# Kernel tuning notes

Hardware: AMD Instinct MI355X
Metric: run time of the kernel (lower is better)

## Reference

```python
import jax, jax.numpy as jnp
import numpy as np

T, N, E = 12, 100000, 3200000
F = H = 64
O, L = 32, 2


def setup_inputs() -> dict:
    key = jax.random.key(0)
    ks = jax.random.split(key, 13)
    sc = 0.08  # keep gate pre-activations in a sane range
    return {
        "x": jax.random.normal(ks[0], (T, N, F), jnp.float32),
        "hidden_states": jax.random.normal(ks[1], (L, N, H), jnp.float32),
        "cell_states": jax.random.normal(ks[2], (L, N, H), jnp.float32),
        "Wx_self": jax.random.normal(ks[3], (L, 4, F, H), jnp.float32) * sc,
        "Wx_neigh": jax.random.normal(ks[4], (L, 4, F, H), jnp.float32) * sc,
        "Wh_self": jax.random.normal(ks[5], (L, 4, H, H), jnp.float32) * sc,
        "Wh_neigh": jax.random.normal(ks[6], (L, 4, H, H), jnp.float32) * sc,
        "w_c": jax.random.normal(ks[7], (L, 3, H), jnp.float32) * sc,  # peephole i,f,o
        "bias": jax.random.normal(ks[8], (L, 4, H), jnp.float32) * sc,  # i,f,c,o
        "Wout": jax.random.normal(ks[9], (H, O), jnp.float32) * sc,
        "bout": jax.random.normal(ks[10], (O,), jnp.float32) * sc,
        "src": jax.random.randint(ks[11], (E,), 0, N, jnp.int32),
        "dst": jax.random.randint(ks[12], (E,), 0, N, jnp.int32),
    }


def reference(x, hidden_states, cell_states, Wx_self, Wx_neigh, Wh_self,
              Wh_neigh, w_c, bias, Wout, bout, src, dst):
    # mean aggregation over incoming edges (DGL copy_u + mean reduce)
    deg = jax.ops.segment_sum(jnp.ones((E,), x.dtype), dst, num_segments=N)
    deg_inv = jnp.where(deg > 0, 1.0 / deg, 0.0)[:, None]  # [N,1]

    def mean_agg(feat):  # [N,D] -> [N,D]
        return jax.ops.segment_sum(feat[src], dst, num_segments=N) * deg_inv

    def gates(feat, agg, Ws, Wn):  # Ws,Wn: [4,D,H] -> [4,N,H]
        return (jnp.einsum('nf,gfh->gnh', feat, Ws)
                + jnp.einsum('nf,gfh->gnh', agg, Wn))

    def step(carry, x_t):
        hs, cs = carry  # [L,N,H] each
        inp = x_t
        new_h, new_c = [], []
        for j in range(L):
            h, c = hs[j], cs[j]
            x_agg = mean_agg(inp)  # reuse_msg_passing: one agg shared by 4 gates
            h_agg = mean_agg(h)
            pre = gates(inp, x_agg, Wx_self[j], Wx_neigh[j]) \
                + gates(h, h_agg, Wh_self[j], Wh_neigh[j])  # [4,N,H]
            i = jax.nn.sigmoid(pre[0] + w_c[j, 0] * c + bias[j, 0])
            f = jax.nn.sigmoid(pre[1] + w_c[j, 1] * c + bias[j, 1])
            c_tilde = jnp.tanh(pre[2] + bias[j, 2])
            nc = f * c + i * c_tilde
            o = jax.nn.sigmoid(pre[3] + w_c[j, 2] * nc + bias[j, 3])
            nh = o * jnp.tanh(nc)
            new_h.append(nh)
            new_c.append(nc)
            inp = nh
        out_t = inp @ Wout + bout  # [N,O]
        return (jnp.stack(new_h), jnp.stack(new_c)), out_t

    (h_f, c_f), outs = jax.lax.scan(step, (hidden_states, cell_states), x)
    return outs, h_f, c_f  # outs: [T,N,O]
```

## Files before the change

kernel.cpp:

```cpp
#include <hip/hip_runtime.h>

#define T_STEPS 12
#define NN 100000
#define EE 3200000
#define HD 64
#define OD 32
#define NBK 391

typedef __attribute__((ext_vector_type(8))) short short8;
typedef __attribute__((ext_vector_type(4))) float f32x4;
typedef __attribute__((ext_vector_type(2))) float f32x2;
typedef unsigned short u16;
typedef unsigned char u8;

__device__ __forceinline__ u16 f2b(float x) {
  union { float f; unsigned u; } v; v.f = x;
  unsigned r = v.u + 0x7FFFu + ((v.u >> 16) & 1u);
  return (u16)(r >> 16);
}
__device__ __forceinline__ u16 f2h(float x) {
  union { _Float16 h; u16 s; } u; u.h = (_Float16)x; return u.s;
}
__device__ __forceinline__ float h2f(u16 s) {
  union { u16 s; _Float16 h; } u; u.s = s; return (float)u.h;
}
__device__ __forceinline__ float sigm(float x) {
  x = fminf(fmaxf(x, -30.f), 30.f);
  return 1.0f / (1.0f + __expf(-x));
}
__device__ __forceinline__ float tanh_f(float x) {
  x = fminf(fmaxf(x, -15.f), 15.f);
  float e = __expf(2.0f * x);
  return (e - 1.0f) / (e + 1.0f);
}

__device__ __forceinline__ uint2 pack8_fp8(const float* f) {
  unsigned lo = 0, hi = 0;
  lo = __builtin_amdgcn_cvt_pk_fp8_f32(f[0], f[1], lo, false);
  lo = __builtin_amdgcn_cvt_pk_fp8_f32(f[2], f[3], lo, true);
  hi = __builtin_amdgcn_cvt_pk_fp8_f32(f[4], f[5], hi, false);
  hi = __builtin_amdgcn_cvt_pk_fp8_f32(f[6], f[7], hi, true);
  return make_uint2(lo, hi);
}
__device__ __forceinline__ u8 f2q(float x) {
  return (u8)(__builtin_amdgcn_cvt_pk_fp8_f32(x, 0.f, 0u, false) & 0xFFu);
}
__device__ __forceinline__ void acc8_fp8(uint2 v, float* a) {
  f32x2 p0 = __builtin_amdgcn_cvt_pk_f32_fp8(v.x, false);
  f32x2 p1 = __builtin_amdgcn_cvt_pk_f32_fp8(v.x, true);
  f32x2 p2 = __builtin_amdgcn_cvt_pk_f32_fp8(v.y, false);
  f32x2 p3 = __builtin_amdgcn_cvt_pk_f32_fp8(v.y, true);
  a[0] += p0[0]; a[1] += p0[1]; a[2] += p1[0]; a[3] += p1[1];
  a[4] += p2[0]; a[5] += p2[1]; a[6] += p3[0]; a[7] += p3[1];
}
__device__ __forceinline__ void dec16_acc2(uint4 q, f32x2* a) {
  a[0] += __builtin_amdgcn_cvt_pk_f32_fp8(q.x, false);
  a[1] += __builtin_amdgcn_cvt_pk_f32_fp8(q.x, true);
  a[2] += __builtin_amdgcn_cvt_pk_f32_fp8(q.y, false);
  a[3] += __builtin_amdgcn_cvt_pk_f32_fp8(q.y, true);
  a[4] += __builtin_amdgcn_cvt_pk_f32_fp8(q.z, false);
  a[5] += __builtin_amdgcn_cvt_pk_f32_fp8(q.z, true);
  a[6] += __builtin_amdgcn_cvt_pk_f32_fp8(q.w, false);
  a[7] += __builtin_amdgcn_cvt_pk_f32_fp8(q.w, true);
}
__device__ __forceinline__ short8 s8_from_fp8(uint2 q) {
  f32x2 p0 = __builtin_amdgcn_cvt_pk_f32_fp8(q.x, false);
  f32x2 p1 = __builtin_amdgcn_cvt_pk_f32_fp8(q.x, true);
  f32x2 p2 = __builtin_amdgcn_cvt_pk_f32_fp8(q.y, false);
  f32x2 p3 = __builtin_amdgcn_cvt_pk_f32_fp8(q.y, true);
  short8 o;
  o[0] = (short)f2b(p0[0]); o[1] = (short)f2b(p0[1]);
  o[2] = (short)f2b(p1[0]); o[3] = (short)f2b(p1[1]);
  o[4] = (short)f2b(p2[0]); o[5] = (short)f2b(p2[1]);
  o[6] = (short)f2b(p3[0]); o[7] = (short)f2b(p3[1]);
  return o;
}
__device__ __forceinline__ short8 s8_from_f32(float4 a, float4 b) {
  short8 o;
  o[0] = (short)f2b(a.x); o[1] = (short)f2b(a.y);
  o[2] = (short)f2b(a.z); o[3] = (short)f2b(a.w);
  o[4] = (short)f2b(b.x); o[5] = (short)f2b(b.y);
  o[6] = (short)f2b(b.z); o[7] = (short)f2b(b.w);
  return o;
}

__global__ __launch_bounds__(256) void k_bhist(const int* __restrict__ dst,
                                               int* __restrict__ bcnt, int E) {
  __shared__ int h[NBK];
  for (int i = threadIdx.x; i < NBK; i += 256) h[i] = 0;
  __syncthreads();
  int base = blockIdx.x * 4096;
#pragma unroll
  for (int i = 0; i < 16; ++i) {
    int e = base + i * 256 + threadIdx.x;
    if (e < E) atomicAdd(&h[dst[e] >> 8], 1);
  }
  __syncthreads();
  for (int i = threadIdx.x; i < NBK; i += 256)
    if (h[i]) atomicAdd(&bcnt[i], h[i]);
}

__global__ __launch_bounds__(512) void k_bscan(const int* __restrict__ bcnt,
                                               int* __restrict__ bcur) {
  __shared__ int buf[512];
  int tid = threadIdx.x;
  int v = (tid < NBK) ? bcnt[tid] : 0;
  buf[tid] = v;
  __syncthreads();
  for (int off = 1; off < 512; off <<= 1) {
    int t = (tid >= off) ? buf[tid - off] : 0;
    __syncthreads();
    buf[tid] += t;
    __syncthreads();
  }
  if (tid < NBK) bcur[tid] = buf[tid] - v;
}

__global__ __launch_bounds__(256) void k_bscatter(const int* __restrict__ src,
                                                  const int* __restrict__ dst,
                                                  int* __restrict__ bcur,
                                                  uint2* __restrict__ binned, int E) {
  __shared__ int h[NBK];
  __shared__ int base[NBK];
  __shared__ int cur[NBK];
  for (int i = threadIdx.x; i < NBK; i += 256) { h[i] = 0; cur[i] = 0; }
  __syncthreads();
  int b0 = blockIdx.x * 4096;
  int d[16], s[16];
#pragma unroll
  for (int i = 0; i < 16; ++i) {
    int e = b0 + i * 256 + threadIdx.x;
    if (e < E) {
      d[i] = dst[e];
      s[i] = src[e];
      atomicAdd(&h[d[i] >> 8], 1);
    } else d[i] = -1;
  }
  __syncthreads();
  for (int i = threadIdx.x; i < NBK; i += 256)
    if (h[i]) base[i] = atomicAdd(&bcur[i], h[i]);
  __syncthreads();
#pragma unroll
  for (int i = 0; i < 16; ++i) {
    if (d[i] >= 0) {
      int bk = d[i] >> 8;
      int r = atomicAdd(&cur[bk], 1);
      binned[base[bk] + r] = make_uint2((unsigned)s[i], (unsigned)d[i]);
    }
  }
}

__global__ __launch_bounds__(256) void k_count2(const uint2* __restrict__ binned,
                                                int* __restrict__ deg, int E) {
  int e = blockIdx.x * 256 + threadIdx.x;
  if (e < E) atomicAdd(&deg[binned[e].y], 1);
}

__global__ __launch_bounds__(1024) void k_scanA(const int* __restrict__ deg,
                                                int* __restrict__ excl,
                                                int* __restrict__ btot, int n) {
  __shared__ int buf[1024];
  int tid = threadIdx.x;
  int i = blockIdx.x * 1024 + tid;
  int v = (i < n) ? deg[i] : 0;
  buf[tid] = v;
  __syncthreads();
  for (int off = 1; off < 1024; off <<= 1) {
    int t = (tid >= off) ? buf[tid - off] : 0;
    __syncthreads();
    buf[tid] += t;
    __syncthreads();
  }
  if (i < n) excl[i] = buf[tid] - v;
  if (tid == 1023) btot[blockIdx.x] = buf[1023];
}

__global__ __launch_bounds__(128) void k_scanB(const int* __restrict__ btot,
                                               int* __restrict__ boffs, int nb) {
  __shared__ int buf[128];
  int tid = threadIdx.x;
  int v = (tid < nb) ? btot[tid] : 0;
  buf[tid] = v;
  __syncthreads();
  for (int off = 1; off < 128; off <<= 1) {
    int t = (tid >= off) ? buf[tid - off] : 0;
    __syncthreads();
    buf[tid] += t;
    __syncthreads();
  }
  if (tid < nb) boffs[tid] = buf[tid] - v;
}

__global__ __launch_bounds__(1024) void k_scanC(const int* __restrict__ deg,
                                                const int* __restrict__ excl,
                                                const int* __restrict__ boffs,
                                                int* __restrict__ row_ptr,
                                                int* __restrict__ cursor,
                                                float* __restrict__ deg_inv, int n) {
  int i = blockIdx.x * 1024 + threadIdx.x;
  if (i < n) {
    int v = excl[i] + boffs[blockIdx.x];
    int d = deg[i];
    row_ptr[i] = v;
    cursor[i] = v;
    deg_inv[i] = d ? (1.0f / (float)d) : 0.0f;
    if (i == n - 1) row_ptr[n] = v + d;
  }
}

__global__ __launch_bounds__(256) void k_scatter2(const uint2* __restrict__ binned,
                                                  int* __restrict__ cursor,
                                                  int* __restrict__ csr, int E) {
  int e = blockIdx.x * 256 + threadIdx.x;
  if (e < E) {
    uint2 p = binned[e];
    int pos = atomicAdd(&cursor[p.y], 1);
    csr[pos] = (int)p.x;
  }
}

__global__ __launch_bounds__(256) void k_prep(const float* __restrict__ Wxs,
                                              const float* __restrict__ Wxn,
                                              const float* __restrict__ Whs,
                                              const float* __restrict__ Whn,
                                              u16* __restrict__ bprep) {
  int idx = blockIdx.x * 256 + threadIdx.x;
  int l = idx >> 16;
  int kb = (idx >> 13) & 7;
  int fi = (idx >> 9) & 15;
  int ln = (idx >> 3) & 63;
  int j = idx & 7;
  int fc = kb * 32 + ((ln >> 4) << 3) + j;
  int g = fi & 3;
  int kk = ((fi >> 2) << 4) + (ln & 15);
  int t = fc >> 6, f = fc & 63;
  const float* tabs[4] = {Wxs, Wxn, Whs, Whn};
  bprep[idx] = f2b(tabs[t][((size_t)(l * 4 + g) * 64 + f) * 64 + kk]);
}

__global__ __launch_bounds__(256) void k_prepw(const float* __restrict__ Wout,
                                               u16* __restrict__ wp) {
  int idx = blockIdx.x * 256 + threadIdx.x;
  int kb = idx >> 10;
  int fi = (idx >> 9) & 1;
  int ln = (idx >> 3) & 63;
  int j = idx & 7;
  int k = kb * 32 + ((ln >> 4) << 3) + j;
  int o = fi * 16 + (ln & 15);
  wp[idx] = f2b(Wout[k * 32 + o]);
}

__global__ __launch_bounds__(256) void k_convxall(const float* __restrict__ x,
                                                  u8* __restrict__ XQ) {
  int tid = blockIdx.x * 256 + threadIdx.x;
  int j = tid & 7;
  int tn = tid >> 3;
  int n = tn % NN;
  int t = tn / NN;
  const float* rp = x + (size_t)tn * 64 + j * 8;
  float4 v0 = *reinterpret_cast<const float4*>(rp);
  float4 v1 = *reinterpret_cast<const float4*>(rp + 4);
  float f[8] = {v0.x, v0.y, v0.z, v0.w, v1.x, v1.y, v1.z, v1.w};
  *reinterpret_cast<uint2*>(XQ + (size_t)n * 768 + t * 64 + j * 8) = pack8_fp8(f);
}

__global__ __launch_bounds__(256) void k_inith(const float* __restrict__ h0,
                                               const float* __restrict__ c0,
                                               u16* __restrict__ H0bf,
                                               u16* __restrict__ L1bf,
                                               u8* __restrict__ HQ,
                                               u16* __restrict__ C16) {
  int idx = blockIdx.x * 256 + threadIdx.x;
  int n = idx >> 3, j = idx & 7;
#pragma unroll
  for (int L = 0; L < 2; ++L) {
    const float* rp = h0 + (size_t)L * NN * 64 + (size_t)n * 64 + j * 8;
    float4 v0 = *reinterpret_cast<const float4*>(rp);
    float4 v1 = *reinterpret_cast<const float4*>(rp + 4);
    float f[8] = {v0.x, v0.y, v0.z, v0.w, v1.x, v1.y, v1.z, v1.w};
    short8 o;
#pragma unroll
    for (int i = 0; i < 8; ++i) o[i] = (short)f2b(f[i]);
    if (L == 0)
      *reinterpret_cast<short8*>(H0bf + (size_t)n * 64 + j * 8) = o;
    else
      *reinterpret_cast<short8*>(L1bf + (size_t)n * 64 + j * 8) = o;
    *reinterpret_cast<uint2*>(HQ + (size_t)n * 128 + L * 64 + j * 8) = pack8_fp8(f);
    const float* cp = c0 + (size_t)L * NN * 64 + (size_t)n * 64 + j * 8;
    float4 c0v = *reinterpret_cast<const float4*>(cp);
    float4 c1v = *reinterpret_cast<const float4*>(cp + 4);
    float cf[8] = {c0v.x, c0v.y, c0v.z, c0v.w, c1v.x, c1v.y, c1v.z, c1v.w};
    short8 oc;
#pragma unroll
    for (int i = 0; i < 8; ++i) oc[i] = (short)f2h(cf[i]);
    *reinterpret_cast<short8*>(C16 + (size_t)L * NN * 64 + (size_t)n * 64 + j * 8) = oc;
  }
}

__global__ __launch_bounds__(256) void k_aggx(const u8* __restrict__ XQ,
                                              const int* __restrict__ row_ptr,
                                              const int* __restrict__ csr,
                                              const float* __restrict__ deg_inv,
                                              u8* __restrict__ AGGXq) {
  int node = blockIdx.x * 4 + (threadIdx.x >> 6);
  int lane = threadIdx.x & 63;
  int g = lane >> 4, m = lane & 15;
  int start = row_ptr[node], end = row_ptr[node + 1];
  f32x2 acc[3][8];
#pragma unroll
  for (int p = 0; p < 3; ++p)
#pragma unroll
    for (int i = 0; i < 8; ++i) acc[p][i] = (f32x2){0.f, 0.f};
  int e = start + g;
  for (; e + 4 < end; e += 8) {
    int s0 = csr[e], s1 = csr[e + 4];
    const u8* r0 = XQ + (size_t)s0 * 768 + m * 16;
    const u8* r1 = XQ + (size_t)s1 * 768 + m * 16;
#pragma unroll
    for (int p = 0; p < 3; ++p) {
      uint4 q0 = *reinterpret_cast<const uint4*>(r0 + p * 256);
      uint4 q1 = *reinterpret_cast<const uint4*>(r1 + p * 256);
      dec16_acc2(q0, acc[p]);
      dec16_acc2(q1, acc[p]);
    }
  }
  if (e < end) {
    int s0 = csr[e];
    const u8* r0 = XQ + (size_t)s0 * 768 + m * 16;
#pragma unroll
    for (int p = 0; p < 3; ++p) {
      uint4 q0 = *reinterpret_cast<const uint4*>(r0 + p * 256);
      dec16_acc2(q0, acc[p]);
    }
  }
#pragma unroll
  for (int off = 16; off < 64; off <<= 1)
#pragma unroll
    for (int p = 0; p < 3; ++p)
#pragma unroll
      for (int i = 0; i < 8; ++i) {
        acc[p][i][0] += __shfl_xor(acc[p][i][0], off);
        acc[p][i][1] += __shfl_xor(acc[p][i][1], off);
      }
  if (g == 0) {
    float sc = deg_inv[node];
#pragma unroll
    for (int p = 0; p < 3; ++p) {
      float f[16];
#pragma unroll
      for (int i = 0; i < 8; ++i) {
        f[i * 2] = acc[p][i][0] * sc;
        f[i * 2 + 1] = acc[p][i][1] * sc;
      }
      uint4 o;
      unsigned w;
      w = 0; w = __builtin_amdgcn_cvt_pk_fp8_f32(f[0], f[1], w, false);
      w = __builtin_amdgcn_cvt_pk_fp8_f32(f[2], f[3], w, true); o.x = w;
      w = 0; w = __builtin_amdgcn_cvt_pk_fp8_f32(f[4], f[5], w, false);
      w = __builtin_amdgcn_cvt_pk_fp8_f32(f[6], f[7], w, true); o.y = w;
      w = 0; w = __builtin_amdgcn_cvt_pk_fp8_f32(f[8], f[9], w, false);
      w = __builtin_amdgcn_cvt_pk_fp8_f32(f[10], f[11], w, true); o.z = w;
      w = 0; w = __builtin_amdgcn_cvt_pk_fp8_f32(f[12], f[13], w, false);
      w = __builtin_amdgcn_cvt_pk_fp8_f32(f[14], f[15], w, true); o.w = w;
      int t = p * 4 + (m >> 2);
      *reinterpret_cast<uint4*>(AGGXq + ((size_t)t * NN + node) * 64 + (m & 3) * 16) = o;
    }
  }
}

__global__ __launch_bounds__(256) void k_agg_pair(const u8* __restrict__ Q,
                                                  const int* __restrict__ row_ptr,
                                                  const int* __restrict__ csr,
                                                  const float* __restrict__ deg_inv,
                                                  u16* __restrict__ out0,
                                                  u16* __restrict__ out1) {
  int node = blockIdx.x * 4 + (threadIdx.x >> 6);
  int lane = threadIdx.x & 63;
  int g = lane >> 4, m = lane & 15;
  int start = row_ptr[node], end = row_ptr[node + 1];
  float a[8] = {0, 0, 0, 0, 0, 0, 0, 0};
  int e = start + g;
  for (; e + 12 < end; e += 16) {
    int s0 = csr[e], s1 = csr[e + 4], s2 = csr[e + 8], s3 = csr[e + 12];
    uint2 v0 = *reinterpret_cast<const uint2*>(Q + (size_t)s0 * 128 + m * 8);
    uint2 v1 = *reinterpret_cast<const uint2*>(Q + (size_t)s1 * 128 + m * 8);
    uint2 v2 = *reinterpret_cast<const uint2*>(Q + (size_t)s2 * 128 + m * 8);
    uint2 v3 = *reinterpret_cast<const uint2*>(Q + (size_t)s3 * 128 + m * 8);
    acc8_fp8(v0, a); acc8_fp8(v1, a); acc8_fp8(v2, a); acc8_fp8(v3, a);
  }
  if (e + 4 < end) {
    int s0 = csr[e], s1 = csr[e + 4];
    uint2 v0 = *reinterpret_cast<const uint2*>(Q + (size_t)s0 * 128 + m * 8);
    uint2 v1 = *reinterpret_cast<const uint2*>(Q + (size_t)s1 * 128 + m * 8);
    acc8_fp8(v0, a); acc8_fp8(v1, a);
    e += 8;
  }
  if (e < end) {
    int s0 = csr[e];
    uint2 v0 = *reinterpret_cast<const uint2*>(Q + (size_t)s0 * 128 + m * 8);
    acc8_fp8(v0, a);
  }
#pragma unroll
  for (int off = 16; off < 64; off <<= 1) {
#pragma unroll
    for (int i = 0; i < 8; ++i) a[i] += __shfl_xor(a[i], off);
  }
  if (g == 0) {
    float sc = deg_inv[node];
    short8 o;
#pragma unroll
    for (int i = 0; i < 8; ++i) o[i] = (short)f2b(a[i] * sc);
    if (m < 8)
      *reinterpret_cast<short8*>(out0 + (size_t)node * 64 + m * 8) = o;
    else
      *reinterpret_cast<short8*>(out1 + (size_t)node * 64 + (m - 8) * 8) = o;
  }
}

__global__ __launch_bounds__(256, 2) void k_gates0(
    const float* __restrict__ xin, const u8* __restrict__ aggxq,
    u16* __restrict__ h0bf, const u16* __restrict__ aggh0,
    u8* __restrict__ hq, u16* __restrict__ c16,
    float* __restrict__ hf32, float* __restrict__ cf32,
    const u16* __restrict__ bprepl,
    const float* __restrict__ wcl, const float* __restrict__ biasl,
    int n_nodes, int wf) {
  const int tid = threadIdx.x;
  const int lane = tid & 63;
  const int w = tid >> 6;
  const int nb = blockIdx.x * 64;
  const int cl = lane & 15;
  const int kg = lane >> 4;

  short8 breg[8][4];
#pragma unroll
  for (int kb = 0; kb < 8; ++kb)
#pragma unroll
    for (int fl = 0; fl < 4; ++fl)
      breg[kb][fl] = *reinterpret_cast<const short8*>(
          bprepl + (kb << 13) + (((w << 2) + fl) << 9) + (lane << 3));

  int gnc[4];
#pragma unroll
  for (int rg = 0; rg < 4; ++rg) {
    int g = nb + rg * 16 + cl;
    gnc[rg] = (g < n_nodes) ? g : (n_nodes - 1);
  }

  f32x4 acc[4][4];
  f32x4 z4 = {0.f, 0.f, 0.f, 0.f};
#pragma unroll
  for (int a = 0; a < 4; ++a)
#pragma unroll
    for (int b = 0; b < 4; ++b) acc[a][b] = z4;

  const int koff = kg << 3;
#pragma unroll
  for (int kb = 0; kb < 8; ++kb) {
    const int idx = ((kb & 1) << 5) + koff;
#pragma unroll
    for (int rg = 0; rg < 4; ++rg) {
      short8 a;
      if (kb < 2) {
        const float* rp = xin + (size_t)gnc[rg] * 64 + idx;
        a = s8_from_f32(*reinterpret_cast<const float4*>(rp),
                        *reinterpret_cast<const float4*>(rp + 4));
      } else if (kb < 4) {
        a = s8_from_fp8(*reinterpret_cast<const uint2*>(aggxq + (size_t)gnc[rg] * 64 + idx));
      } else if (kb < 6) {
        a = *reinterpret_cast<const short8*>(h0bf + (size_t)gnc[rg] * 64 + idx);
      } else {
        a = *reinterpret_cast<const short8*>(aggh0 + (size_t)gnc[rg] * 64 + idx);
      }
      acc[rg][0] = __builtin_amdgcn_mfma_f32_16x16x32_bf16(a, breg[kb][0], acc[rg][0], 0, 0, 0);
      acc[rg][1] = __builtin_amdgcn_mfma_f32_16x16x32_bf16(a, breg[kb][1], acc[rg][1], 0, 0, 0);
      acc[rg][2] = __builtin_amdgcn_mfma_f32_16x16x32_bf16(a, breg[kb][2], acc[rg][2], 0, 0, 0);
      acc[rg][3] = __builtin_amdgcn_mfma_f32_16x16x32_bf16(a, breg[kb][3], acc[rg][3], 0, 0, 0);
    }
  }
  __syncthreads();

  const int k = (w << 4) + cl;
  const float wci = wcl[k], wcf = wcl[64 + k], wco = wcl[128 + k];
  const float bi = biasl[k], bfg = biasl[64 + k], bc = biasl[128 + k], bo = biasl[192 + k];
#pragma unroll
  for (int rg = 0; rg < 4; ++rg) {
#pragma unroll
    for (int r = 0; r < 4; ++r) {
      int n = nb + rg * 16 + kg * 4 + r;
      if (n < n_nodes) {
        size_t off = (size_t)n * 64 + k;
        float c_old = h2f(c16[off]);
        float ig = sigm(acc[rg][0][r] + wci * c_old + bi);
        float fg = sigm(acc[rg][1][r] + wcf * c_old + bfg);
        float ct = tanh_f(acc[rg][2][r] + bc);
        float nc = fg * c_old + ig * ct;
        float og = sigm(acc[rg][3][r] + wco * nc + bo);
        float nh = og * tanh_f(nc);
        c16[off] = f2h(nc);
        h0bf[off] = f2b(nh);
        hq[(size_t)n * 128 + k] = f2q(nh);
        if (wf) { hf32[off] = nh; cf32[off] = nc; }
      }
    }
  }
}

__global__ __launch_bounds__(256, 2) void k_gates1(
    const u16* __restrict__ h0bf, const u16* __restrict__ aggh0,
    const u16* __restrict__ aggh1,
    u16* __restrict__ l1bf, u8* __restrict__ hq, u16* __restrict__ c16,
    float* __restrict__ hf32, float* __restrict__ cf32,
    const u16* __restrict__ bprepl,
    const float* __restrict__ wcl, const float* __restrict__ biasl,
    const u16* __restrict__ wproj, const float* __restrict__ boutp,
    float* __restrict__ outp, int n_nodes, int wf) {
  __shared__ u16 Hsm[64 * 64];
  const int tid = threadIdx.x;
  const int lane = tid & 63;
  const int w = tid >> 6;
  const int nb = blockIdx.x * 64;
  const int cl = lane & 15;
  const int kg = lane >> 4;

  short8 breg[8][4];
#pragma unroll
  for (int kb = 0; kb < 8; ++kb)
#pragma unroll
    for (int fl = 0; fl < 4; ++fl)
      breg[kb][fl] = *reinterpret_cast<const short8*>(
          bprepl + (kb << 13) + (((w << 2) + fl) << 9) + (lane << 3));

  int gnc[4];
#pragma unroll
  for (int rg = 0; rg < 4; ++rg) {
    int g = nb + rg * 16 + cl;
    gnc[rg] = (g < n_nodes) ? g : (n_nodes - 1);
  }

  f32x4 acc[4][4];
  f32x4 z4 = {0.f, 0.f, 0.f, 0.f};
#pragma unroll
  for (int a = 0; a < 4; ++a)
#pragma unroll
    for (int b = 0; b < 4; ++b) acc[a][b] = z4;

  const int koff = kg << 3;
#pragma unroll
  for (int kb = 0; kb < 8; ++kb) {
    const int idx = ((kb & 1) << 5) + koff;
#pragma unroll
    for (int rg = 0; rg < 4; ++rg) {
      short8 a;
      if (kb < 2) {
        a = *reinterpret_cast<const short8*>(h0bf + (size_t)gnc[rg] * 64 + idx);
      } else if (kb < 4) {
        a = *reinterpret_cast<const short8*>(aggh0 + (size_t)gnc[rg] * 64 + idx);
      } else if (kb < 6) {
        a = *reinterpret_cast<const short8*>(l1bf + (size_t)gnc[rg] * 64 + idx);
      } else {
        a = *reinterpret_cast<const short8*>(aggh1 + (size_t)gnc[rg] * 64 + idx);
      }
      acc[rg][0] = __builtin_amdgcn_mfma_f32_16x16x32_bf16(a, breg[kb][0], acc[rg][0], 0, 0, 0);
      acc[rg][1] = __builtin_amdgcn_mfma_f32_16x16x32_bf16(a, breg[kb][1], acc[rg][1], 0, 0, 0);
      acc[rg][2] = __builtin_amdgcn_mfma_f32_16x16x32_bf16(a, breg[kb][2], acc[rg][2], 0, 0, 0);
      acc[rg][3] = __builtin_amdgcn_mfma_f32_16x16x32_bf16(a, breg[kb][3], acc[rg][3], 0, 0, 0);
    }
  }
  __syncthreads();

  const int k = (w << 4) + cl;
  const float wci = wcl[k], wcf = wcl[64 + k], wco = wcl[128 + k];
  const float bi = biasl[k], bfg = biasl[64 + k], bc = biasl[128 + k], bo = biasl[192 + k];
#pragma unroll
  for (int rg = 0; rg < 4; ++rg) {
#pragma unroll
    for (int r = 0; r < 4; ++r) {
      int n = nb + rg * 16 + kg * 4 + r;
      if (n < n_nodes) {
        size_t off = (size_t)n * 64 + k;
        float c_old = h2f(c16[off]);
        float ig = sigm(acc[rg][0][r] + wci * c_old + bi);
        float fg = sigm(acc[rg][1][r] + wcf * c_old + bfg);
        float ct = tanh_f(acc[rg][2][r] + bc);
        float nc = fg * c_old + ig * ct;
        float og = sigm(acc[rg][3][r] + wco * nc + bo);
        float nh = og * tanh_f(nc);
        c16[off] = f2h(nc);
        u16 hb = f2b(nh);
        l1bf[off] = hb;
        hq[(size_t)n * 128 + 64 + k] = f2q(nh);
        Hsm[(rg * 16 + kg * 4 + r) * 64 + k] = hb;
        if (wf) { hf32[off] = nh; cf32[off] = nc; }
      }
    }
  }

  __syncthreads();
  short8 bw[2][2];
#pragma unroll
  for (int kb = 0; kb < 2; ++kb)
#pragma unroll
    for (int fi = 0; fi < 2; ++fi)
      bw[kb][fi] = *reinterpret_cast<const short8*>(wproj + (((kb * 2 + fi) * 64 + lane) << 3));
  short8 a0 = *reinterpret_cast<const short8*>(&Hsm[(w * 16 + cl) * 64 + kg * 8]);
  short8 a1 = *reinterpret_cast<const short8*>(&Hsm[(w * 16 + cl) * 64 + 32 + kg * 8]);
  f32x4 p0 = z4, p1 = z4;
  p0 = __builtin_amdgcn_mfma_f32_16x16x32_bf16(a0, bw[0][0], p0, 0, 0, 0);
  p0 = __builtin_amdgcn_mfma_f32_16x16x32_bf16(a1, bw[1][0], p0, 0, 0, 0);
  p1 = __builtin_amdgcn_mfma_f32_16x16x32_bf16(a0, bw[0][1], p1, 0, 0, 0);
  p1 = __builtin_amdgcn_mfma_f32_16x16x32_bf16(a1, bw[1][1], p1, 0, 0, 0);
  const float bo0 = boutp[cl], bo1 = boutp[16 + cl];
#pragma unroll
  for (int r = 0; r < 4; ++r) {
    int n = nb + w * 16 + kg * 4 + r;
    if (n < n_nodes) {
      outp[(size_t)n * OD + cl] = p0[r] + bo0;
      outp[(size_t)n * OD + 16 + cl] = p1[r] + bo1;
    }
  }
}

extern "C" void kernel_launch(void* const* d_in, const int* in_sizes, int n_in,
                              void* d_out, int out_size, void* d_ws, size_t ws_size,
                              hipStream_t stream) {
  const float* x = (const float*)d_in[0];
  const float* h0 = (const float*)d_in[1];
  const float* c0 = (const float*)d_in[2];
  const float* Wxs = (const float*)d_in[3];
  const float* Wxn = (const float*)d_in[4];
  const float* Whs = (const float*)d_in[5];
  const float* Whn = (const float*)d_in[6];
  const float* wc = (const float*)d_in[7];
  const float* bias = (const float*)d_in[8];
  const float* Wout = (const float*)d_in[9];
  const float* bout = (const float*)d_in[10];
  const int* src = (const int*)d_in[11];
  const int* dst = (const int*)d_in[12];

  float* out = (float*)d_out;
  float* outs = out;
  float* hstate = out + (size_t)T_STEPS * NN * OD;
  float* cstate = hstate + (size_t)2 * NN * HD;

  char* p = (char*)d_ws;
  auto alloc = [&](size_t bytes) {
    char* r = p;
    p += (bytes + 255) & ~(size_t)255;
    return r;
  };
  int* csr = (int*)alloc((size_t)EE * 4);
  u8* XQ = (u8*)alloc((size_t)NN * 768);
  uint2* binned = (uint2*)XQ;
  u8* AGGXq = (u8*)alloc((size_t)T_STEPS * NN * 64);
  int* row_ptr = (int*)alloc((size_t)(NN + 1) * 4);
  int* cursor = (int*)alloc((size_t)NN * 4);
  int* deg = (int*)alloc((size_t)NN * 4);
  int* excl = (int*)alloc((size_t)NN * 4);
  int* btot = (int*)alloc(128 * 4);
  int* boffs = (int*)alloc(128 * 4);
  int* bcnt = (int*)alloc(NBK * 4);
  int* bcur = (int*)alloc(NBK * 4);
  float* deg_inv = (float*)alloc((size_t)NN * 4);
  u16* H0bf = (u16*)alloc((size_t)NN * 64 * 2);
  u16* L1bf = (u16*)alloc((size_t)NN * 64 * 2);
  u8* HQ = (u8*)alloc((size_t)NN * 128);
  u16* AGGH0 = (u16*)alloc((size_t)NN * 64 * 2);
  u16* AGGH1 = (u16*)alloc((size_t)NN * 64 * 2);
  u16* C16 = (u16*)alloc((size_t)2 * NN * 64 * 2);
  u16* bprep = (u16*)alloc((size_t)2 * 65536 * 2);
  u16* wprep = (u16*)alloc((size_t)2048 * 2);

  const int nscan = (NN + 1023) / 1024;
  const int nchunk = (EE + 4095) / 4096;

  hipMemsetAsync(deg, 0, (size_t)NN * 4, stream);
  hipMemsetAsync(bcnt, 0, (size_t)NBK * 4, stream);
  k_bhist<<<nchunk, 256, 0, stream>>>(dst, bcnt, EE);
  k_bscan<<<1, 512, 0, stream>>>(bcnt, bcur);
  k_bscatter<<<nchunk, 256, 0, stream>>>(src, dst, bcur, binned, EE);
  k_count2<<<(EE + 255) / 256, 256, 0, stream>>>(binned, deg, EE);
  k_scanA<<<nscan, 1024, 0, stream>>>(deg, excl, btot, NN);
  k_scanB<<<1, 128, 0, stream>>>(btot, boffs, nscan);
  k_scanC<<<nscan, 1024, 0, stream>>>(deg, excl, boffs, row_ptr, cursor, deg_inv, NN);
  k_scatter2<<<(EE + 255) / 256, 256, 0, stream>>>(binned, cursor, csr, EE);
  k_prep<<<512, 256, 0, stream>>>(Wxs, Wxn, Whs, Whn, bprep);
  k_prepw<<<8, 256, 0, stream>>>(Wout, wprep);
  k_convxall<<<(T_STEPS * NN * 8 + 255) / 256, 256, 0, stream>>>(x, XQ);
  k_inith<<<NN * 8 / 256, 256, 0, stream>>>(h0, c0, H0bf, L1bf, HQ, C16);
  k_aggx<<<(NN + 3) / 4, 256, 0, stream>>>(XQ, row_ptr, csr, deg_inv, AGGXq);
  k_agg_pair<<<(NN + 3) / 4, 256, 0, stream>>>(HQ, row_ptr, csr, deg_inv, AGGH0, AGGH1);

  for (int t = 0; t < T_STEPS; ++t) {
    int wf = (t == T_STEPS - 1) ? 1 : 0;
    k_gates0<<<(NN + 63) / 64, 256, 0, stream>>>(
        x + (size_t)t * NN * HD, AGGXq + (size_t)t * NN * 64,
        H0bf, AGGH0, HQ, C16, hstate, cstate, bprep, wc, bias, NN, wf);
    k_agg_pair<<<(NN + 3) / 4, 256, 0, stream>>>(HQ, row_ptr, csr, deg_inv, AGGH0, AGGH1);
    k_gates1<<<(NN + 63) / 64, 256, 0, stream>>>(
        H0bf, AGGH0, AGGH1, L1bf, HQ, C16 + (size_t)NN * 64,
        hstate + (size_t)NN * HD, cstate + (size_t)NN * HD,
        bprep + 65536, wc + 192, bias + 256,
        wprep, bout, outs + (size_t)t * NN * OD, NN, wf);
  }
}
```

Before: 2.984 ms.

## Build CSR per destination bucket in one kernel; split x aggregation by time group

```diff
diff --git a/kernel.cpp b/kernel.cpp
--- a/kernel.cpp
+++ b/kernel.cpp
@@ -101,6 +101,7 @@
 }
 
 __global__ __launch_bounds__(512) void k_bscan(const int* __restrict__ bcnt,
+                                               int* __restrict__ bbase,
                                                int* __restrict__ bcur) {
   __shared__ int buf[512];
   int tid = threadIdx.x;
@@ -113,7 +114,11 @@
     buf[tid] += t;
     __syncthreads();
   }
-  if (tid < NBK) bcur[tid] = buf[tid] - v;
+  if (tid < NBK) {
+    int e = buf[tid] - v;
+    bbase[tid] = e;
+    bcur[tid] = e;
+  }
 }
 
 __global__ __launch_bounds__(256) void k_bscatter(const int* __restrict__ src,
@@ -150,72 +155,45 @@
   }
 }
 
-__global__ __launch_bounds__(256) void k_count2(const uint2* __restrict__ binned,
-                                                int* __restrict__ deg, int E) {
-  int e = blockIdx.x * 256 + threadIdx.x;
-  if (e < E) atomicAdd(&deg[binned[e].y], 1);
-}
-
-__global__ __launch_bounds__(1024) void k_scanA(const int* __restrict__ deg,
-                                                int* __restrict__ excl,
-                                                int* __restrict__ btot, int n) {
-  __shared__ int buf[1024];
-  int tid = threadIdx.x;
-  int i = blockIdx.x * 1024 + tid;
-  int v = (i < n) ? deg[i] : 0;
+__global__ __launch_bounds__(256) void k_bsort(const uint2* __restrict__ binned,
+                                               const int* __restrict__ bbase,
+                                               const int* __restrict__ bcnt,
+                                               int* __restrict__ csr,
+                                               int* __restrict__ row_ptr,
+                                               float* __restrict__ deg_inv, int n) {
+  __shared__ int cnt[256];
+  __shared__ int buf[256];
+  __shared__ int cur[256];
+  int b = blockIdx.x, tid = threadIdx.x;
+  int ebase = bbase[b];
+  int ecnt = bcnt[b];
+  cnt[tid] = 0;
+  __syncthreads();
+  for (int i = tid; i < ecnt; i += 256)
+    atomicAdd(&cnt[binned[ebase + i].y & 255], 1);
+  __syncthreads();
+  int v = cnt[tid];
   buf[tid] = v;
   __syncthreads();
-  for (int off = 1; off < 1024; off <<= 1) {
+  for (int off = 1; off < 256; off <<= 1) {
     int t = (tid >= off) ? buf[tid - off] : 0;
     __syncthreads();
     buf[tid] += t;
     __syncthreads();
   }
-  if (i < n) excl[i] = buf[tid] - v;
-  if (tid == 1023) btot[blockIdx.x] = buf[1023];
-}
-
-__global__ __launch_bounds__(128) void k_scanB(const int* __restrict__ btot,
-                                               int* __restrict__ boffs, int nb) {
-  __shared__ int buf[128];
-  int tid = threadIdx.x;
-  int v = (tid < nb) ? btot[tid] : 0;
-  buf[tid] = v;
-  __syncthreads();
-  for (int off = 1; off < 128; off <<= 1) {
-    int t = (tid >= off) ? buf[tid - off] : 0;
-    __syncthreads();
-    buf[tid] += t;
-    __syncthreads();
-  }
-  if (tid < nb) boffs[tid] = buf[tid] - v;
-}
-
-__global__ __launch_bounds__(1024) void k_scanC(const int* __restrict__ deg,
-                                                const int* __restrict__ excl,
-                                                const int* __restrict__ boffs,
-                                                int* __restrict__ row_ptr,
-                                                int* __restrict__ cursor,
-                                                float* __restrict__ deg_inv, int n) {
-  int i = blockIdx.x * 1024 + threadIdx.x;
-  if (i < n) {
-    int v = excl[i] + boffs[blockIdx.x];
-    int d = deg[i];
-    row_ptr[i] = v;
-    cursor[i] = v;
-    deg_inv[i] = d ? (1.0f / (float)d) : 0.0f;
-    if (i == n - 1) row_ptr[n] = v + d;
-  }
-}
-
-__global__ __launch_bounds__(256) void k_scatter2(const uint2* __restrict__ binned,
-                                                  int* __restrict__ cursor,
-                                                  int* __restrict__ csr, int E) {
-  int e = blockIdx.x * 256 + threadIdx.x;
-  if (e < E) {
-    uint2 p = binned[e];
-    int pos = atomicAdd(&cursor[p.y], 1);
-    csr[pos] = (int)p.x;
+  int excl = buf[tid] - v;
+  int node = b * 256 + tid;
+  if (node < n) {
+    row_ptr[node] = ebase + excl;
+    deg_inv[node] = v ? (1.0f / (float)v) : 0.0f;
+  }
+  if (b == NBK - 1 && tid == 0) row_ptr[n] = ebase + ecnt;
+  cur[tid] = excl;
+  __syncthreads();
+  for (int i = tid; i < ecnt; i += 256) {
+    uint2 pr = binned[ebase + i];
+    int pos = atomicAdd(&cur[pr.y & 255], 1);
+    csr[ebase + pos] = (int)pr.x;
   }
 }
 
@@ -303,68 +281,62 @@
                                               const float* __restrict__ deg_inv,
                                               u8* __restrict__ AGGXq) {
   int node = blockIdx.x * 4 + (threadIdx.x >> 6);
+  int p = blockIdx.y;
   int lane = threadIdx.x & 63;
   int g = lane >> 4, m = lane & 15;
   int start = row_ptr[node], end = row_ptr[node + 1];
-  f32x2 acc[3][8];
-#pragma unroll
-  for (int p = 0; p < 3; ++p)
-#pragma unroll
-    for (int i = 0; i < 8; ++i) acc[p][i] = (f32x2){0.f, 0.f};
+  const size_t poff = (size_t)p * 256 + m * 16;
+  f32x2 a[8];
+#pragma unroll
+  for (int i = 0; i < 8; ++i) a[i] = (f32x2){0.f, 0.f};
   int e = start + g;
-  for (; e + 4 < end; e += 8) {
+  for (; e + 12 < end; e += 16) {
+    int s0 = csr[e], s1 = csr[e + 4], s2 = csr[e + 8], s3 = csr[e + 12];
+    uint4 q0 = *reinterpret_cast<const uint4*>(XQ + (size_t)s0 * 768 + poff);
+    uint4 q1 = *reinterpret_cast<const uint4*>(XQ + (size_t)s1 * 768 + poff);
+    uint4 q2 = *reinterpret_cast<const uint4*>(XQ + (size_t)s2 * 768 + poff);
+    uint4 q3 = *reinterpret_cast<const uint4*>(XQ + (size_t)s3 * 768 + poff);
+    dec16_acc2(q0, a); dec16_acc2(q1, a); dec16_acc2(q2, a); dec16_acc2(q3, a);
+  }
+  if (e + 4 < end) {
     int s0 = csr[e], s1 = csr[e + 4];
-    const u8* r0 = XQ + (size_t)s0 * 768 + m * 16;
-    const u8* r1 = XQ + (size_t)s1 * 768 + m * 16;
-#pragma unroll
-    for (int p = 0; p < 3; ++p) {
-      uint4 q0 = *reinterpret_cast<const uint4*>(r0 + p * 256);
-      uint4 q1 = *reinterpret_cast<const uint4*>(r1 + p * 256);
-      dec16_acc2(q0, acc[p]);
-      dec16_acc2(q1, acc[p]);
-    }
+    uint4 q0 = *reinterpret_cast<const uint4*>(XQ + (size_t)s0 * 768 + poff);
+    uint4 q1 = *reinterpret_cast<const uint4*>(XQ + (size_t)s1 * 768 + poff);
+    dec16_acc2(q0, a); dec16_acc2(q1, a);
+    e += 8;
   }
   if (e < end) {
     int s0 = csr[e];
-    const u8* r0 = XQ + (size_t)s0 * 768 + m * 16;
-#pragma unroll
-    for (int p = 0; p < 3; ++p) {
-      uint4 q0 = *reinterpret_cast<const uint4*>(r0 + p * 256);
-      dec16_acc2(q0, acc[p]);
-    }
+    uint4 q0 = *reinterpret_cast<const uint4*>(XQ + (size_t)s0 * 768 + poff);
+    dec16_acc2(q0, a);
   }
 #pragma unroll
   for (int off = 16; off < 64; off <<= 1)
 #pragma unroll
-    for (int p = 0; p < 3; ++p)
-#pragma unroll
-      for (int i = 0; i < 8; ++i) {
-        acc[p][i][0] += __shfl_xor(acc[p][i][0], off);
-        acc[p][i][1] += __shfl_xor(acc[p][i][1], off);
-      }
+    for (int i = 0; i < 8; ++i) {
+      a[i][0] += __shfl_xor(a[i][0], off);
+      a[i][1] += __shfl_xor(a[i][1], off);
+    }
   if (g == 0) {
     float sc = deg_inv[node];
-#pragma unroll
-    for (int p = 0; p < 3; ++p) {
-      float f[16];
-#pragma unroll
-      for (int i = 0; i < 8; ++i) {
-        f[i * 2] = acc[p][i][0] * sc;
-        f[i * 2 + 1] = acc[p][i][1] * sc;
-      }
-      uint4 o;
-      unsigned w;
-      w = 0; w = __builtin_amdgcn_cvt_pk_fp8_f32(f[0], f[1], w, false);
-      w = __builtin_amdgcn_cvt_pk_fp8_f32(f[2], f[3], w, true); o.x = w;
-      w = 0; w = __builtin_amdgcn_cvt_pk_fp8_f32(f[4], f[5], w, false);
-      w = __builtin_amdgcn_cvt_pk_fp8_f32(f[6], f[7], w, true); o.y = w;
-      w = 0; w = __builtin_amdgcn_cvt_pk_fp8_f32(f[8], f[9], w, false);
-      w = __builtin_amdgcn_cvt_pk_fp8_f32(f[10], f[11], w, true); o.z = w;
-      w = 0; w = __builtin_amdgcn_cvt_pk_fp8_f32(f[12], f[13], w, false);
-      w = __builtin_amdgcn_cvt_pk_fp8_f32(f[14], f[15], w, true); o.w = w;
-      int t = p * 4 + (m >> 2);
-      *reinterpret_cast<uint4*>(AGGXq + ((size_t)t * NN + node) * 64 + (m & 3) * 16) = o;
-    }
+    float f[16];
+#pragma unroll
+    for (int i = 0; i < 8; ++i) {
+      f[i * 2] = a[i][0] * sc;
+      f[i * 2 + 1] = a[i][1] * sc;
+    }
+    uint4 o;
+    unsigned w;
+    w = 0; w = __builtin_amdgcn_cvt_pk_fp8_f32(f[0], f[1], w, false);
+    w = __builtin_amdgcn_cvt_pk_fp8_f32(f[2], f[3], w, true); o.x = w;
+    w = 0; w = __builtin_amdgcn_cvt_pk_fp8_f32(f[4], f[5], w, false);
+    w = __builtin_amdgcn_cvt_pk_fp8_f32(f[6], f[7], w, true); o.y = w;
+    w = 0; w = __builtin_amdgcn_cvt_pk_fp8_f32(f[8], f[9], w, false);
+    w = __builtin_amdgcn_cvt_pk_fp8_f32(f[10], f[11], w, true); o.z = w;
+    w = 0; w = __builtin_amdgcn_cvt_pk_fp8_f32(f[12], f[13], w, false);
+    w = __builtin_amdgcn_cvt_pk_fp8_f32(f[14], f[15], w, true); o.w = w;
+    int t = p * 4 + (m >> 2);
+    *reinterpret_cast<uint4*>(AGGXq + ((size_t)t * NN + node) * 64 + (m & 3) * 16) = o;
   }
 }
 
@@ -654,12 +626,8 @@
   uint2* binned = (uint2*)XQ;
   u8* AGGXq = (u8*)alloc((size_t)T_STEPS * NN * 64);
   int* row_ptr = (int*)alloc((size_t)(NN + 1) * 4);
-  int* cursor = (int*)alloc((size_t)NN * 4);
-  int* deg = (int*)alloc((size_t)NN * 4);
-  int* excl = (int*)alloc((size_t)NN * 4);
-  int* btot = (int*)alloc(128 * 4);
-  int* boffs = (int*)alloc(128 * 4);
   int* bcnt = (int*)alloc(NBK * 4);
+  int* bbase = (int*)alloc(NBK * 4);
   int* bcur = (int*)alloc(NBK * 4);
   float* deg_inv = (float*)alloc((size_t)NN * 4);
   u16* H0bf = (u16*)alloc((size_t)NN * 64 * 2);
@@ -671,24 +639,21 @@
   u16* bprep = (u16*)alloc((size_t)2 * 65536 * 2);
   u16* wprep = (u16*)alloc((size_t)2048 * 2);
 
-  const int nscan = (NN + 1023) / 1024;
   const int nchunk = (EE + 4095) / 4096;
 
-  hipMemsetAsync(deg, 0, (size_t)NN * 4, stream);
   hipMemsetAsync(bcnt, 0, (size_t)NBK * 4, stream);
   k_bhist<<<nchunk, 256, 0, stream>>>(dst, bcnt, EE);
-  k_bscan<<<1, 512, 0, stream>>>(bcnt, bcur);
+  k_bscan<<<1, 512, 0, stream>>>(bcnt, bbase, bcur);
   k_bscatter<<<nchunk, 256, 0, stream>>>(src, dst, bcur, binned, EE);
-  k_count2<<<(EE + 255) / 256, 256, 0, stream>>>(binned, deg, EE);
-  k_scanA<<<nscan, 1024, 0, stream>>>(deg, excl, btot, NN);
-  k_scanB<<<1, 128, 0, stream>>>(btot, boffs, nscan);
-  k_scanC<<<nscan, 1024, 0, stream>>>(deg, excl, boffs, row_ptr, cursor, deg_inv, NN);
-  k_scatter2<<<(EE + 255) / 256, 256, 0, stream>>>(binned, cursor, csr, EE);
+  k_bsort<<<NBK, 256, 0, stream>>>(binned, bbase, bcnt, csr, row_ptr, deg_inv, NN);
   k_prep<<<512, 256, 0, stream>>>(Wxs, Wxn, Whs, Whn, bprep);
   k_prepw<<<8, 256, 0, stream>>>(Wout, wprep);
   k_convxall<<<(T_STEPS * NN * 8 + 255) / 256, 256, 0, stream>>>(x, XQ);
   k_inith<<<NN * 8 / 256, 256, 0, stream>>>(h0, c0, H0bf, L1bf, HQ, C16);
-  k_aggx<<<(NN + 3) / 4, 256, 0, stream>>>(XQ, row_ptr, csr, deg_inv, AGGXq);
+  {
+    dim3 g((NN + 3) / 4, 3);
+    k_aggx<<<g, 256, 0, stream>>>(XQ, row_ptr, csr, deg_inv, AGGXq);
+  }
   k_agg_pair<<<(NN + 3) / 4, 256, 0, stream>>>(HQ, row_ptr, csr, deg_inv, AGGH0, AGGH1);
 
   for (int t = 0; t < T_STEPS; ++t) {
```

Result: faster. 2.887 ms (median of 2 runs) (-3.3%).
